# Optimization experiments

Hardware: AMD Instinct MI355X
Metric: run time of the kernel (lower is better)

Reference implementation:

```python
import jax, jax.numpy as jnp
import numpy as np

B, T, C = 8, 1024, 768
NH = 12
HD = C // NH  # 64


def setup_inputs() -> dict:
    key = jax.random.key(0)
    k1, k2, k3 = jax.random.split(key, 3)
    x = jax.random.normal(k1, (B, T, C), dtype=jnp.float32)
    w_attn = jax.random.normal(k2, (C, 3 * C), dtype=jnp.float32) * 0.02
    b_attn = jnp.zeros((3 * C,), dtype=jnp.float32)
    w_proj = jax.random.normal(k3, (C, C), dtype=jnp.float32) * 0.02
    b_proj = jnp.zeros((C,), dtype=jnp.float32)
    return {"x": x, "w_attn": w_attn, "b_attn": b_attn, "w_proj": w_proj, "b_proj": b_proj}


def reference(x, w_attn, b_attn, w_proj, b_proj):
    Bb, Tt, Cc = x.shape
    qkv = x @ w_attn + b_attn  # [B,T,3C]
    q, k, v = jnp.split(qkv, [Cc, 2 * Cc], axis=-1)
    # [B, NH, T, HD]
    q = q.reshape(Bb, Tt, NH, HD).swapaxes(1, 2)
    k = k.reshape(Bb, Tt, NH, HD).swapaxes(1, 2)
    v = v.reshape(Bb, Tt, NH, HD).swapaxes(1, 2)
    scale = 1.0 / jnp.sqrt(jnp.asarray(HD, dtype=x.dtype))
    att = jnp.einsum("bhqd,bhkd->bhqk", q, k) * scale  # [B,NH,T,T]
    causal = jnp.tril(jnp.ones((Tt, Tt), dtype=bool))[None, None]
    att = jnp.where(causal, att, jnp.asarray(-jnp.inf, dtype=att.dtype))
    att = jax.nn.softmax(att, axis=-1)
    y = jnp.einsum("bhqk,bhkd->bhqd", att, v)  # [B,NH,T,HD]
    y = y.swapaxes(1, 2).reshape(Bb, Tt, Cc)
    return y @ w_proj + b_proj
```

## Files before the change

### kernel.cpp

```cpp
#include <hip/hip_runtime.h>
#include <cstdint>
#include <cstddef>

typedef __attribute__((ext_vector_type(8))) short short8;
typedef __attribute__((ext_vector_type(4))) float f32x4;
typedef __attribute__((ext_vector_type(4))) unsigned short u16x4;

#define ASYNC16(gp, lp) \
  __builtin_amdgcn_global_load_lds((const __attribute__((address_space(1))) unsigned int*)(gp), \
                                   (__attribute__((address_space(3))) unsigned int*)(lp), 16, 0, 0)

__device__ __forceinline__ unsigned short f2b(float f) {
  union { float f; unsigned int u; } c; c.f = f;
  unsigned int u = c.u;
  return (unsigned short)((u + 0x7fffu + ((u >> 16) & 1u)) >> 16);
}


__global__ __launch_bounds__(256) void prep(
    const float* __restrict__ x, unsigned short* __restrict__ xb,
    const float* __restrict__ w_attn, unsigned short* __restrict__ waT,
    const float* __restrict__ w_proj, unsigned short* __restrict__ wpT) {
  __shared__ unsigned short Ts[64][65];
  const int bb = blockIdx.x;
  const int tid = threadIdx.x;
  if (bb < 3072) {
    int i = (bb * 256 + tid) * 8;
    float4 v0 = *(const float4*)(x + i);
    float4 v1 = *(const float4*)(x + i + 4);
    short8 v;
    ((unsigned short*)&v)[0] = f2b(v0.x);
    ((unsigned short*)&v)[1] = f2b(v0.y);
    ((unsigned short*)&v)[2] = f2b(v0.z);
    ((unsigned short*)&v)[3] = f2b(v0.w);
    ((unsigned short*)&v)[4] = f2b(v1.x);
    ((unsigned short*)&v)[5] = f2b(v1.y);
    ((unsigned short*)&v)[6] = f2b(v1.z);
    ((unsigned short*)&v)[7] = f2b(v1.w);
    *(short8*)(xb + i) = v;
    return;
  }
  const float* W; unsigned short* WT; int Kd, Nd, n0, k0;
  if (bb < 3504) {
    int t = bb - 3072; W = w_attn; WT = waT; Kd = 768; Nd = 2304;
    n0 = (t % 36) * 64; k0 = (t / 36) * 64;
  } else {
    int t = bb - 3504; W = w_proj; WT = wpT; Kd = 768; Nd = 768;
    n0 = (t % 12) * 64; k0 = (t / 12) * 64;
  }
  for (int idx = tid; idx < 4096; idx += 256) {
    int lr = idx >> 6, lc = idx & 63;
    Ts[lr][lc] = f2b(W[(size_t)(k0 + lr) * Nd + n0 + lc]);
  }
  __syncthreads();
  for (int idx = tid; idx < 4096; idx += 256) {
    int nr = idx >> 6, kc = idx & 63;
    WT[(size_t)(n0 + nr) * Kd + k0 + kc] = Ts[kc][nr];
  }
}


__global__ __launch_bounds__(256, 2) void gemm_qkv(
    const unsigned short* __restrict__ A,
    const unsigned short* __restrict__ Bt,
    const float* __restrict__ bias,
    unsigned short* __restrict__ q,
    unsigned short* __restrict__ k,
    unsigned short* __restrict__ vT)
{
  __shared__ unsigned short As[2][128 * 64];
  __shared__ unsigned short Bs[2][128 * 64];
  const int tid = threadIdx.x;
  const int w = tid >> 6, lane = tid & 63;
  const int wm = w >> 1, wn = w & 1;
  const int lr = lane & 15, lq = lane >> 4;

  const int bid = blockIdx.x;
  const int xcd = bid & 7;
  const int local = bid >> 3;
  const int ty = local >> 3;
  const int tx = xcd * 8 + (local & 7);
  const int m0 = tx * 128, n0 = ty * 128;
  const f32x4 fzero = {0.f, 0.f, 0.f, 0.f};

  f32x4 acc[4][4];
  for (int i = 0; i < 4; ++i) for (int j = 0; j < 4; ++j) acc[i][j] = fzero;

  const int trow = tid >> 3;
  const int tcol = (tid & 7) ^ (trow & 7);
  const unsigned short* Asrc = A + (size_t)(m0 + trow) * 768 + tcol * 8;
  const unsigned short* Bsrc = Bt + (size_t)(n0 + trow) * 768 + tcol * 8;
  const int dst0 = tid * 16;

#define STAGE_QKV(s, bidx) do { \
    const unsigned short* as_ = Asrc + (s) * 64; \
    const unsigned short* bs_ = Bsrc + (s) * 64; \
    ASYNC16(as_,            (char*)As[bidx] + dst0); \
    ASYNC16(as_ + 32 * 768, (char*)As[bidx] + dst0 + 4096); \
    ASYNC16(as_ + 64 * 768, (char*)As[bidx] + dst0 + 8192); \
    ASYNC16(as_ + 96 * 768, (char*)As[bidx] + dst0 + 12288); \
    ASYNC16(bs_,            (char*)Bs[bidx] + dst0); \
    ASYNC16(bs_ + 32 * 768, (char*)Bs[bidx] + dst0 + 4096); \
    ASYNC16(bs_ + 64 * 768, (char*)Bs[bidx] + dst0 + 8192); \
    ASYNC16(bs_ + 96 * 768, (char*)Bs[bidx] + dst0 + 12288); \
  } while (0)

  STAGE_QKV(0, 0);

  const int swz = (lq ^ (lr & 7)) * 16;
  const int arow = (wm * 64 + lr) * 128;
  const int brow = (wn * 64 + lr) * 128;

  for (int s = 0; s < 12; ++s) {
    __builtin_amdgcn_s_barrier();
    if (s + 1 < 12) {
      STAGE_QKV(s + 1, (s + 1) & 1);
      asm volatile("s_waitcnt vmcnt(8)" ::: "memory");
    } else {
      asm volatile("s_waitcnt vmcnt(0)" ::: "memory");
    }
    __builtin_amdgcn_s_barrier();
    __builtin_amdgcn_sched_barrier(0);
    const char* asb = (const char*)As[s & 1];
    const char* bsb = (const char*)Bs[s & 1];
    for (int ks = 0; ks < 2; ++ks) {
      const int cb = swz ^ (ks << 6);
      short8 a[4], b[4];
      for (int i = 0; i < 4; ++i)
        a[i] = *(const short8*)(asb + arow + i * 2048 + cb);
      for (int j = 0; j < 4; ++j)
        b[j] = *(const short8*)(bsb + brow + j * 2048 + cb);
      for (int i = 0; i < 4; ++i)
        for (int j = 0; j < 4; ++j)
          acc[i][j] = __builtin_amdgcn_mfma_f32_16x16x32_bf16(a[i], b[j], acc[i][j], 0, 0, 0);
    }
  }
#undef STAGE_QKV

  const int colbase = n0 + wn * 64;
  const int sec = colbase / 768;
  const float QSCALE = 0.18033688011112042f;
  for (int j = 0; j < 4; ++j) {
    int col = colbase + j * 16 + lr;
    int cc = col - sec * 768;
    int h = cc >> 6, d = cc & 63;
    float bv = bias[col];
    for (int i = 0; i < 4; ++i) {
      int row0 = m0 + wm * 64 + i * 16 + lq * 4;
      int bidx = row0 >> 10, t0 = row0 & 1023;
      int bh = bidx * 12 + h;
      if (sec == 0) {
        for (int r = 0; r < 4; ++r)
          q[((size_t)bh * 1024 + t0 + r) * 64 + d] = f2b((acc[i][j][r] + bv) * QSCALE);
      } else if (sec == 1) {
        for (int r = 0; r < 4; ++r)
          k[((size_t)bh * 1024 + t0 + r) * 64 + d] = f2b(acc[i][j][r] + bv);
      } else {
        u16x4 pv;
        pv[0] = f2b(acc[i][j][0] + bv);
        pv[1] = f2b(acc[i][j][1] + bv);
        pv[2] = f2b(acc[i][j][2] + bv);
        pv[3] = f2b(acc[i][j][3] + bv);
        *(u16x4*)(vT + ((size_t)bh * 64 + d) * 1024 + t0) = pv;
      }
    }
  }
}


__global__ __launch_bounds__(256, 3) void attn(
    const unsigned short* __restrict__ q,
    const unsigned short* __restrict__ kk,
    const unsigned short* __restrict__ vT,
    unsigned short* __restrict__ y)
{
  __shared__ __attribute__((aligned(16))) char smem[46080];
  unsigned short* KsB0 = (unsigned short*)smem;
  unsigned short* KsB1 = (unsigned short*)(smem + 9216);
  unsigned short* VtB0 = (unsigned short*)(smem + 18432);
  unsigned short* VtB1 = (unsigned short*)(smem + 27648);
  unsigned short* Ps   = (unsigned short*)(smem + 36864);
  unsigned short* Qs   = (unsigned short*)smem;

  const int tid = threadIdx.x;
  const int w = tid >> 6, lane = tid & 63;
  const int lr = lane & 15, lq = lane >> 4;

  const int bid = blockIdx.x;
  const int xcd = bid & 7;
  const int local = bid >> 3;
  const int bh = xcd + 8 * (local >> 3);
  const int qp = local & 7;
  const int qt1 = 15 - qp;
  const int b = bh / 12, h = bh - b * 12;
  const f32x4 fzero = {0.f, 0.f, 0.f, 0.f};

  unsigned short* Pw = Ps + w * 16 * 72;
  const unsigned short* kbase = kk + (size_t)bh * 65536;
  const unsigned short* vbase = vT + (size_t)bh * 65536;

  const int c0 = tid, c1 = tid + 256;
  short8 kreg[2], vreg[2];
  kreg[0] = *(const short8*)(kbase + (size_t)c0 * 8);
  kreg[1] = *(const short8*)(kbase + (size_t)c1 * 8);
  vreg[0] = *(const short8*)(vbase + (size_t)(c0 >> 3) * 1024 + (c0 & 7) * 8);
  vreg[1] = *(const short8*)(vbase + (size_t)(c1 >> 3) * 1024 + (c1 & 7) * 8);

  {
    const unsigned short* qa = q + ((size_t)bh * 1024 + qp * 64) * 64;
    const unsigned short* qb = q + ((size_t)bh * 1024 + qt1 * 64) * 64;
    for (int c = tid; c < 512; c += 256) {
      int row = c >> 3, d0 = (c & 7) * 8;
      *(short8*)(Qs + row * 72 + d0)        = *(const short8*)(qa + (size_t)c * 8);
      *(short8*)(Qs + (row + 64) * 72 + d0) = *(const short8*)(qb + (size_t)c * 8);
    }
  }
  __syncthreads();
  short8 qf0[2], qf1[2];
  for (int ks = 0; ks < 2; ++ks) {
    qf0[ks] = *(const short8*)(Qs + (w * 16 + lr) * 72 + ks * 32 + lq * 8);
    qf1[ks] = *(const short8*)(Qs + (64 + w * 16 + lr) * 72 + ks * 32 + lq * 8);
  }
  __syncthreads();

  const int wo0 = (c0 >> 3) * 72 + (c0 & 7) * 8;
  const int wo1 = (c1 >> 3) * 72 + (c1 & 7) * 8;

  *(short8*)(KsB0 + wo0) = kreg[0];
  *(short8*)(KsB0 + wo1) = kreg[1];
  *(short8*)(VtB0 + wo0) = vreg[0];
  *(short8*)(VtB0 + wo1) = vreg[1];

  const int nkt = qt1 + 1;
  {
    const unsigned short* kp = kbase + 4096;
    const unsigned short* vp = vbase + 64;
    kreg[0] = *(const short8*)(kp + (size_t)c0 * 8);
    kreg[1] = *(const short8*)(kp + (size_t)c1 * 8);
    vreg[0] = *(const short8*)(vp + (size_t)(c0 >> 3) * 1024 + (c0 & 7) * 8);
    vreg[1] = *(const short8*)(vp + (size_t)(c1 >> 3) * 1024 + (c1 & 7) * 8);
  }

  f32x4 o0[4], o1[4];
  float l0[4], l1[4];
  for (int jd = 0; jd < 4; ++jd) { o0[jd] = fzero; o1[jd] = fzero; }
  for (int r = 0; r < 4; ++r) { l0[r] = 0.0f; l1[r] = 0.0f; }

  for (int kt = 0; kt < nkt; ++kt) {
    __syncthreads();
    const unsigned short* Ks = (kt & 1) ? KsB1 : KsB0;
    const unsigned short* Vt = (kt & 1) ? VtB1 : VtB0;
    if (kt + 1 < nkt) {
      unsigned short* Ksn = (kt & 1) ? KsB0 : KsB1;
      unsigned short* Vtn = (kt & 1) ? VtB0 : VtB1;
      *(short8*)(Ksn + wo0) = kreg[0];
      *(short8*)(Ksn + wo1) = kreg[1];
      *(short8*)(Vtn + wo0) = vreg[0];
      *(short8*)(Vtn + wo1) = vreg[1];
      if (kt + 2 < nkt) {
        const unsigned short* kp = kbase + (size_t)(kt + 2) * 4096;
        const unsigned short* vp = vbase + (size_t)(kt + 2) * 64;
        kreg[0] = *(const short8*)(kp + (size_t)c0 * 8);
        kreg[1] = *(const short8*)(kp + (size_t)c1 * 8);
        vreg[0] = *(const short8*)(vp + (size_t)(c0 >> 3) * 1024 + (c0 & 7) * 8);
        vreg[1] = *(const short8*)(vp + (size_t)(c1 >> 3) * 1024 + (c1 & 7) * 8);
      }
    }

    const bool act0 = (kt <= qp);

    f32x4 s0[4], s1[4];
    for (int j = 0; j < 4; ++j) { s0[j] = fzero; s1[j] = fzero; }
    {
      short8 bk[2][4];
      for (int ks = 0; ks < 2; ++ks)
        for (int j = 0; j < 4; ++j)
          bk[ks][j] = *(const short8*)(Ks + (j * 16 + lr) * 72 + ks * 32 + lq * 8);
      __builtin_amdgcn_s_setprio(1);
      if (act0) {
        for (int ks = 0; ks < 2; ++ks)
          for (int j = 0; j < 4; ++j)
            s0[j] = __builtin_amdgcn_mfma_f32_16x16x32_bf16(qf0[ks], bk[ks][j], s0[j], 0, 0, 0);
      }
      for (int ks = 0; ks < 2; ++ks)
        for (int j = 0; j < 4; ++j)
          s1[j] = __builtin_amdgcn_mfma_f32_16x16x32_bf16(qf1[ks], bk[ks][j], s1[j], 0, 0, 0);
      __builtin_amdgcn_s_setprio(0);
    }

    short8 bvr[2][4];
    for (int ks = 0; ks < 2; ++ks)
      for (int jd = 0; jd < 4; ++jd)
        bvr[ks][jd] = *(const short8*)(Vt + (jd * 16 + lr) * 72 + ks * 32 + lq * 8);

    if (act0) {
      if (kt == qp) {
        int rowt = w * 16 + lq * 4;
        for (int j = 0; j < 4; ++j) {
          int colt = j * 16 + lr;
          for (int r = 0; r < 4; ++r)
            if (colt > rowt + r) s0[j][r] = -1e30f;
        }
      }
      for (int r = 0; r < 4; ++r) {
        int prow = (lq * 4 + r) * 72;
        float acc = 0.0f;
        for (int j = 0; j < 4; ++j) {
          float p = __builtin_amdgcn_exp2f(s0[j][r]);
          acc += p;
          union { float f; unsigned int u; } cv; cv.f = p;
          Pw[prow + j * 16 + lr] = (unsigned short)((cv.u + 0x8000u) >> 16);
        }
        l0[r] += acc;
      }
      __builtin_amdgcn_s_setprio(1);
      for (int ks = 0; ks < 2; ++ks) {
        short8 ap = *(const short8*)(Pw + lr * 72 + ks * 32 + lq * 8);
        for (int jd = 0; jd < 4; ++jd)
          o0[jd] = __builtin_amdgcn_mfma_f32_16x16x32_bf16(ap, bvr[ks][jd], o0[jd], 0, 0, 0);
      }
      __builtin_amdgcn_s_setprio(0);
    }

    {
      if (kt == qt1) {
        int rowt = w * 16 + lq * 4;
        for (int j = 0; j < 4; ++j) {
          int colt = j * 16 + lr;
          for (int r = 0; r < 4; ++r)
            if (colt > rowt + r) s1[j][r] = -1e30f;
        }
      }
      for (int r = 0; r < 4; ++r) {
        int prow = (lq * 4 + r) * 72;
        float acc = 0.0f;
        for (int j = 0; j < 4; ++j) {
          float p = __builtin_amdgcn_exp2f(s1[j][r]);
          acc += p;
          union { float f; unsigned int u; } cv; cv.f = p;
          Pw[prow + j * 16 + lr] = (unsigned short)((cv.u + 0x8000u) >> 16);
        }
        l1[r] += acc;
      }
      __builtin_amdgcn_s_setprio(1);
      for (int ks = 0; ks < 2; ++ks) {
        short8 ap = *(const short8*)(Pw + lr * 72 + ks * 32 + lq * 8);
        for (int jd = 0; jd < 4; ++jd)
          o1[jd] = __builtin_amdgcn_mfma_f32_16x16x32_bf16(ap, bvr[ks][jd], o1[jd], 0, 0, 0);
      }
      __builtin_amdgcn_s_setprio(0);
    }
  }

  for (int r = 0; r < 4; ++r) {
    float a0 = l0[r], a1 = l1[r];
    for (int off = 1; off < 16; off <<= 1) {
      a0 += __shfl_xor(a0, off, 16);
      a1 += __shfl_xor(a1, off, 16);
    }
    l0[r] = 1.0f / a0;
    l1[r] = 1.0f / a1;
  }
  int t0 = qp * 64 + w * 16 + lq * 4;
  int t1 = qt1 * 64 + w * 16 + lq * 4;
  for (int jd = 0; jd < 4; ++jd) {
    int d = jd * 16 + lr;
    for (int r = 0; r < 4; ++r) {
      y[((size_t)b * 1024 + t0 + r) * 768 + h * 64 + d] = f2b(o0[jd][r] * l0[r]);
      y[((size_t)b * 1024 + t1 + r) * 768 + h * 64 + d] = f2b(o1[jd][r] * l1[r]);
    }
  }
}


__global__ __launch_bounds__(256, 3) void gemm_proj(
    const unsigned short* __restrict__ A,
    const unsigned short* __restrict__ Bt,
    const float* __restrict__ bias,
    float* __restrict__ out)
{
  __shared__ unsigned short As[2][64 * 64];
  __shared__ unsigned short Bs[2][128 * 64];
  const int tid = threadIdx.x;
  const int w = tid >> 6, lane = tid & 63;
  const int wm = w >> 1, wn = w & 1;
  const int lr = lane & 15, lq = lane >> 4;

  const int bid = blockIdx.x;
  const int xcd = bid & 7;
  const int local = bid >> 3;
  const int ty = local >> 4;
  const int tx = xcd * 16 + (local & 15);
  const int m0 = tx * 64, n0 = ty * 128;
  const f32x4 fzero = {0.f, 0.f, 0.f, 0.f};

  f32x4 acc[2][4];
  for (int i = 0; i < 2; ++i) for (int j = 0; j < 4; ++j) acc[i][j] = fzero;

  const int trow = tid >> 3;
  const int tcol = (tid & 7) ^ (trow & 7);
  const unsigned short* Asrc = A + (size_t)(m0 + trow) * 768 + tcol * 8;
  const unsigned short* Bsrc = Bt + (size_t)(n0 + trow) * 768 + tcol * 8;
  const int dst0 = tid * 16;

#define STAGE_PROJ(s, bidx) do { \
    const unsigned short* as_ = Asrc + (s) * 64; \
    const unsigned short* bs_ = Bsrc + (s) * 64; \
    ASYNC16(as_,            (char*)As[bidx] + dst0); \
    ASYNC16(as_ + 32 * 768, (char*)As[bidx] + dst0 + 4096); \
    ASYNC16(bs_,            (char*)Bs[bidx] + dst0); \
    ASYNC16(bs_ + 32 * 768, (char*)Bs[bidx] + dst0 + 4096); \
    ASYNC16(bs_ + 64 * 768, (char*)Bs[bidx] + dst0 + 8192); \
    ASYNC16(bs_ + 96 * 768, (char*)Bs[bidx] + dst0 + 12288); \
  } while (0)

  STAGE_PROJ(0, 0);

  const int swz = (lq ^ (lr & 7)) * 16;
  const int arow = (wm * 32 + lr) * 128;
  const int brow = (wn * 64 + lr) * 128;

  for (int s = 0; s < 12; ++s) {
    __builtin_amdgcn_s_barrier();
    if (s + 1 < 12) {
      STAGE_PROJ(s + 1, (s + 1) & 1);
      asm volatile("s_waitcnt vmcnt(6)" ::: "memory");
    } else {
      asm volatile("s_waitcnt vmcnt(0)" ::: "memory");
    }
    __builtin_amdgcn_s_barrier();
    __builtin_amdgcn_sched_barrier(0);
    const char* asb = (const char*)As[s & 1];
    const char* bsb = (const char*)Bs[s & 1];
    for (int ks = 0; ks < 2; ++ks) {
      const int cb = swz ^ (ks << 6);
      short8 a[2], b[4];
      for (int i = 0; i < 2; ++i)
        a[i] = *(const short8*)(asb + arow + i * 2048 + cb);
      for (int j = 0; j < 4; ++j)
        b[j] = *(const short8*)(bsb + brow + j * 2048 + cb);
      for (int i = 0; i < 2; ++i)
        for (int j = 0; j < 4; ++j)
          acc[i][j] = __builtin_amdgcn_mfma_f32_16x16x32_bf16(a[i], b[j], acc[i][j], 0, 0, 0);
    }
  }
#undef STAGE_PROJ

  for (int j = 0; j < 4; ++j) {
    int col = n0 + wn * 64 + j * 16 + lr;
    float bv = bias[col];
    for (int i = 0; i < 2; ++i) {
      int row0 = m0 + wm * 32 + i * 16 + lq * 4;
      for (int r = 0; r < 4; ++r)
        out[(size_t)(row0 + r) * 768 + col] = acc[i][j][r] + bv;
    }
  }
}


extern "C" void kernel_launch(void* const* d_in, const int* in_sizes, int n_in,
                              void* d_out, int out_size, void* d_ws, size_t ws_size,
                              hipStream_t stream) {
  const float* x      = (const float*)d_in[0];
  const float* w_attn = (const float*)d_in[1];
  const float* b_attn = (const float*)d_in[2];
  const float* w_proj = (const float*)d_in[3];
  const float* b_proj = (const float*)d_in[4];
  float* out = (float*)d_out;

  char* p = (char*)d_ws;
  unsigned short* xb  = (unsigned short*)p; p += (size_t)8192 * 768 * 2;
  unsigned short* waT = (unsigned short*)p; p += (size_t)2304 * 768 * 2;
  unsigned short* wpT = (unsigned short*)p; p += (size_t)768 * 768 * 2;
  unsigned short* qb  = (unsigned short*)p; p += (size_t)96 * 1024 * 64 * 2;
  unsigned short* kb  = (unsigned short*)p; p += (size_t)96 * 1024 * 64 * 2;
  unsigned short* vTb = (unsigned short*)p; p += (size_t)96 * 64 * 1024 * 2;
  unsigned short* yb  = (unsigned short*)p; p += (size_t)8192 * 768 * 2;

  prep<<<3648, 256, 0, stream>>>(x, xb, w_attn, waT, w_proj, wpT);
  gemm_qkv<<<1152, 256, 0, stream>>>(xb, waT, b_attn, qb, kb, vTb);
  attn<<<768, 256, 0, stream>>>(qb, kb, vTb, yb);
  gemm_proj<<<768, 256, 0, stream>>>(yb, wpT, b_proj, out);
}
```

Before: 174.2 us.

## Split paired causal query tiles into one tile per block, single-buffer V

The attention kernel no longer pairs a short and a long causal query tile in one block; each block now handles a single 64-row query tile, so the grid doubles to 1536 blocks. V tiles are single-buffered and an extra barrier separates the softmax from the PV product, which cuts LDS use and allows four blocks per CU instead of three. The trade-off is that work per block now varies with the tile index, so load balance depends on the hardware scheduler. Each K/V tile is also loaded once per query tile rather than once per pair, and the extra barrier per iteration adds synchronisation.

```diff
diff --git a/kernel.cpp b/kernel.cpp
--- a/kernel.cpp
+++ b/kernel.cpp
@@ -168,18 +168,17 @@
 }
 
 
-__global__ __launch_bounds__(256, 3) void attn(
+__global__ __launch_bounds__(256, 4) void attn(
     const unsigned short* __restrict__ q,
     const unsigned short* __restrict__ kk,
     const unsigned short* __restrict__ vT,
     unsigned short* __restrict__ y)
 {
-  __shared__ __attribute__((aligned(16))) char smem[46080];
+  __shared__ __attribute__((aligned(16))) char smem[36864];
   unsigned short* KsB0 = (unsigned short*)smem;
   unsigned short* KsB1 = (unsigned short*)(smem + 9216);
-  unsigned short* VtB0 = (unsigned short*)(smem + 18432);
-  unsigned short* VtB1 = (unsigned short*)(smem + 27648);
-  unsigned short* Ps   = (unsigned short*)(smem + 36864);
+  unsigned short* Vt   = (unsigned short*)(smem + 18432);
+  unsigned short* Ps   = (unsigned short*)(smem + 27648);
   unsigned short* Qs   = (unsigned short*)smem;
 
   const int tid = threadIdx.x;
@@ -189,17 +188,20 @@
   const int bid = blockIdx.x;
   const int xcd = bid & 7;
   const int local = bid >> 3;
-  const int bh = xcd + 8 * (local >> 3);
-  const int qp = local & 7;
-  const int qt1 = 15 - qp;
+  const int bh = xcd + 8 * (local >> 4);
+  const int s = local & 15;
   const int b = bh / 12, h = bh - b * 12;
   const f32x4 fzero = {0.f, 0.f, 0.f, 0.f};
 
   unsigned short* Pw = Ps + w * 16 * 72;
   const unsigned short* kbase = kk + (size_t)bh * 65536;
   const unsigned short* vbase = vT + (size_t)bh * 65536;
+  const int nkt = s + 1;
 
   const int c0 = tid, c1 = tid + 256;
+  const int wo0 = (c0 >> 3) * 72 + (c0 & 7) * 8;
+  const int wo1 = (c1 >> 3) * 72 + (c1 & 7) * 8;
+
   short8 kreg[2], vreg[2];
   kreg[0] = *(const short8*)(kbase + (size_t)c0 * 8);
   kreg[1] = *(const short8*)(kbase + (size_t)c1 * 8);
@@ -207,168 +209,101 @@
   vreg[1] = *(const short8*)(vbase + (size_t)(c1 >> 3) * 1024 + (c1 & 7) * 8);
 
   {
-    const unsigned short* qa = q + ((size_t)bh * 1024 + qp * 64) * 64;
-    const unsigned short* qb = q + ((size_t)bh * 1024 + qt1 * 64) * 64;
+    const unsigned short* qa = q + ((size_t)bh * 1024 + s * 64) * 64;
     for (int c = tid; c < 512; c += 256) {
       int row = c >> 3, d0 = (c & 7) * 8;
-      *(short8*)(Qs + row * 72 + d0)        = *(const short8*)(qa + (size_t)c * 8);
-      *(short8*)(Qs + (row + 64) * 72 + d0) = *(const short8*)(qb + (size_t)c * 8);
+      *(short8*)(Qs + row * 72 + d0) = *(const short8*)(qa + (size_t)c * 8);
     }
   }
   __syncthreads();
-  short8 qf0[2], qf1[2];
-  for (int ks = 0; ks < 2; ++ks) {
-    qf0[ks] = *(const short8*)(Qs + (w * 16 + lr) * 72 + ks * 32 + lq * 8);
-    qf1[ks] = *(const short8*)(Qs + (64 + w * 16 + lr) * 72 + ks * 32 + lq * 8);
-  }
+  short8 qf[2];
+  qf[0] = *(const short8*)(Qs + (w * 16 + lr) * 72 + lq * 8);
+  qf[1] = *(const short8*)(Qs + (w * 16 + lr) * 72 + 32 + lq * 8);
   __syncthreads();
-
-  const int wo0 = (c0 >> 3) * 72 + (c0 & 7) * 8;
-  const int wo1 = (c1 >> 3) * 72 + (c1 & 7) * 8;
 
   *(short8*)(KsB0 + wo0) = kreg[0];
   *(short8*)(KsB0 + wo1) = kreg[1];
-  *(short8*)(VtB0 + wo0) = vreg[0];
-  *(short8*)(VtB0 + wo1) = vreg[1];
-
-  const int nkt = qt1 + 1;
-  {
-    const unsigned short* kp = kbase + 4096;
-    const unsigned short* vp = vbase + 64;
-    kreg[0] = *(const short8*)(kp + (size_t)c0 * 8);
-    kreg[1] = *(const short8*)(kp + (size_t)c1 * 8);
-    vreg[0] = *(const short8*)(vp + (size_t)(c0 >> 3) * 1024 + (c0 & 7) * 8);
-    vreg[1] = *(const short8*)(vp + (size_t)(c1 >> 3) * 1024 + (c1 & 7) * 8);
-  }
-
-  f32x4 o0[4], o1[4];
-  float l0[4], l1[4];
-  for (int jd = 0; jd < 4; ++jd) { o0[jd] = fzero; o1[jd] = fzero; }
-  for (int r = 0; r < 4; ++r) { l0[r] = 0.0f; l1[r] = 0.0f; }
+  if (nkt > 1) {
+    kreg[0] = *(const short8*)(kbase + 4096 + (size_t)c0 * 8);
+    kreg[1] = *(const short8*)(kbase + 4096 + (size_t)c1 * 8);
+  }
+
+  f32x4 o[4];
+  float l[4];
+  for (int jd = 0; jd < 4; ++jd) o[jd] = fzero;
+  for (int r = 0; r < 4; ++r) l[r] = 0.0f;
 
   for (int kt = 0; kt < nkt; ++kt) {
     __syncthreads();
-    const unsigned short* Ks = (kt & 1) ? KsB1 : KsB0;
-    const unsigned short* Vt = (kt & 1) ? VtB1 : VtB0;
+    *(short8*)(Vt + wo0) = vreg[0];
+    *(short8*)(Vt + wo1) = vreg[1];
     if (kt + 1 < nkt) {
-      unsigned short* Ksn = (kt & 1) ? KsB0 : KsB1;
-      unsigned short* Vtn = (kt & 1) ? VtB0 : VtB1;
-      *(short8*)(Ksn + wo0) = kreg[0];
-      *(short8*)(Ksn + wo1) = kreg[1];
-      *(short8*)(Vtn + wo0) = vreg[0];
-      *(short8*)(Vtn + wo1) = vreg[1];
+      unsigned short* Kn = (kt & 1) ? KsB0 : KsB1;
+      *(short8*)(Kn + wo0) = kreg[0];
+      *(short8*)(Kn + wo1) = kreg[1];
+      const unsigned short* vp = vbase + (size_t)(kt + 1) * 64;
+      vreg[0] = *(const short8*)(vp + (size_t)(c0 >> 3) * 1024 + (c0 & 7) * 8);
+      vreg[1] = *(const short8*)(vp + (size_t)(c1 >> 3) * 1024 + (c1 & 7) * 8);
       if (kt + 2 < nkt) {
         const unsigned short* kp = kbase + (size_t)(kt + 2) * 4096;
-        const unsigned short* vp = vbase + (size_t)(kt + 2) * 64;
         kreg[0] = *(const short8*)(kp + (size_t)c0 * 8);
         kreg[1] = *(const short8*)(kp + (size_t)c1 * 8);
-        vreg[0] = *(const short8*)(vp + (size_t)(c0 >> 3) * 1024 + (c0 & 7) * 8);
-        vreg[1] = *(const short8*)(vp + (size_t)(c1 >> 3) * 1024 + (c1 & 7) * 8);
-      }
-    }
-
-    const bool act0 = (kt <= qp);
-
-    f32x4 s0[4], s1[4];
-    for (int j = 0; j < 4; ++j) { s0[j] = fzero; s1[j] = fzero; }
-    {
-      short8 bk[2][4];
-      for (int ks = 0; ks < 2; ++ks)
-        for (int j = 0; j < 4; ++j)
-          bk[ks][j] = *(const short8*)(Ks + (j * 16 + lr) * 72 + ks * 32 + lq * 8);
-      __builtin_amdgcn_s_setprio(1);
-      if (act0) {
-        for (int ks = 0; ks < 2; ++ks)
-          for (int j = 0; j < 4; ++j)
-            s0[j] = __builtin_amdgcn_mfma_f32_16x16x32_bf16(qf0[ks], bk[ks][j], s0[j], 0, 0, 0);
-      }
-      for (int ks = 0; ks < 2; ++ks)
-        for (int j = 0; j < 4; ++j)
-          s1[j] = __builtin_amdgcn_mfma_f32_16x16x32_bf16(qf1[ks], bk[ks][j], s1[j], 0, 0, 0);
-      __builtin_amdgcn_s_setprio(0);
-    }
-
-    short8 bvr[2][4];
+      }
+    }
+
+    const unsigned short* Ks = (kt & 1) ? KsB1 : KsB0;
+    f32x4 sv[4];
+    for (int j = 0; j < 4; ++j) sv[j] = fzero;
+    __builtin_amdgcn_s_setprio(1);
     for (int ks = 0; ks < 2; ++ks)
-      for (int jd = 0; jd < 4; ++jd)
-        bvr[ks][jd] = *(const short8*)(Vt + (jd * 16 + lr) * 72 + ks * 32 + lq * 8);
-
-    if (act0) {
-      if (kt == qp) {
-        int rowt = w * 16 + lq * 4;
-        for (int j = 0; j < 4; ++j) {
-          int colt = j * 16 + lr;
-          for (int r = 0; r < 4; ++r)
-            if (colt > rowt + r) s0[j][r] = -1e30f;
-        }
-      }
-      for (int r = 0; r < 4; ++r) {
-        int prow = (lq * 4 + r) * 72;
-        float acc = 0.0f;
-        for (int j = 0; j < 4; ++j) {
-          float p = __builtin_amdgcn_exp2f(s0[j][r]);
-          acc += p;
-          union { float f; unsigned int u; } cv; cv.f = p;
-          Pw[prow + j * 16 + lr] = (unsigned short)((cv.u + 0x8000u) >> 16);
-        }
-        l0[r] += acc;
-      }
-      __builtin_amdgcn_s_setprio(1);
-      for (int ks = 0; ks < 2; ++ks) {
-        short8 ap = *(const short8*)(Pw + lr * 72 + ks * 32 + lq * 8);
-        for (int jd = 0; jd < 4; ++jd)
-          o0[jd] = __builtin_amdgcn_mfma_f32_16x16x32_bf16(ap, bvr[ks][jd], o0[jd], 0, 0, 0);
-      }
-      __builtin_amdgcn_s_setprio(0);
-    }
-
-    {
-      if (kt == qt1) {
-        int rowt = w * 16 + lq * 4;
-        for (int j = 0; j < 4; ++j) {
-          int colt = j * 16 + lr;
-          for (int r = 0; r < 4; ++r)
-            if (colt > rowt + r) s1[j][r] = -1e30f;
-        }
-      }
-      for (int r = 0; r < 4; ++r) {
-        int prow = (lq * 4 + r) * 72;
-        float acc = 0.0f;
-        for (int j = 0; j < 4; ++j) {
-          float p = __builtin_amdgcn_exp2f(s1[j][r]);
-          acc += p;
-          union { float f; unsigned int u; } cv; cv.f = p;
-          Pw[prow + j * 16 + lr] = (unsigned short)((cv.u + 0x8000u) >> 16);
-        }
-        l1[r] += acc;
-      }
-      __builtin_amdgcn_s_setprio(1);
-      for (int ks = 0; ks < 2; ++ks) {
-        short8 ap = *(const short8*)(Pw + lr * 72 + ks * 32 + lq * 8);
-        for (int jd = 0; jd < 4; ++jd)
-          o1[jd] = __builtin_amdgcn_mfma_f32_16x16x32_bf16(ap, bvr[ks][jd], o1[jd], 0, 0, 0);
-      }
-      __builtin_amdgcn_s_setprio(0);
-    }
+      for (int j = 0; j < 4; ++j) {
+        short8 bk = *(const short8*)(Ks + (j * 16 + lr) * 72 + ks * 32 + lq * 8);
+        sv[j] = __builtin_amdgcn_mfma_f32_16x16x32_bf16(qf[ks], bk, sv[j], 0, 0, 0);
+      }
+    __builtin_amdgcn_s_setprio(0);
+
+    if (kt == s) {
+      int rowt = w * 16 + lq * 4;
+      for (int j = 0; j < 4; ++j) {
+        int colt = j * 16 + lr;
+        for (int r = 0; r < 4; ++r)
+          if (colt > rowt + r) sv[j][r] = -1e30f;
+      }
+    }
+    for (int r = 0; r < 4; ++r) {
+      int prow = (lq * 4 + r) * 72;
+      float acc = 0.0f;
+      for (int j = 0; j < 4; ++j) {
+        float p = __builtin_amdgcn_exp2f(sv[j][r]);
+        acc += p;
+        union { float f; unsigned int u; } cv; cv.f = p;
+        Pw[prow + j * 16 + lr] = (unsigned short)((cv.u + 0x8000u) >> 16);
+      }
+      l[r] += acc;
+    }
+    __syncthreads();
+    __builtin_amdgcn_s_setprio(1);
+    for (int ks = 0; ks < 2; ++ks) {
+      short8 ap = *(const short8*)(Pw + lr * 72 + ks * 32 + lq * 8);
+      for (int jd = 0; jd < 4; ++jd) {
+        short8 bv = *(const short8*)(Vt + (jd * 16 + lr) * 72 + ks * 32 + lq * 8);
+        o[jd] = __builtin_amdgcn_mfma_f32_16x16x32_bf16(ap, bv, o[jd], 0, 0, 0);
+      }
+    }
+    __builtin_amdgcn_s_setprio(0);
   }
 
   for (int r = 0; r < 4; ++r) {
-    float a0 = l0[r], a1 = l1[r];
-    for (int off = 1; off < 16; off <<= 1) {
+    float a0 = l[r];
+    for (int off = 1; off < 16; off <<= 1)
       a0 += __shfl_xor(a0, off, 16);
-      a1 += __shfl_xor(a1, off, 16);
-    }
-    l0[r] = 1.0f / a0;
-    l1[r] = 1.0f / a1;
-  }
-  int t0 = qp * 64 + w * 16 + lq * 4;
-  int t1 = qt1 * 64 + w * 16 + lq * 4;
+    l[r] = 1.0f / a0;
+  }
+  int t0 = s * 64 + w * 16 + lq * 4;
   for (int jd = 0; jd < 4; ++jd) {
     int d = jd * 16 + lr;
-    for (int r = 0; r < 4; ++r) {
-      y[((size_t)b * 1024 + t0 + r) * 768 + h * 64 + d] = f2b(o0[jd][r] * l0[r]);
-      y[((size_t)b * 1024 + t1 + r) * 768 + h * 64 + d] = f2b(o1[jd][r] * l1[r]);
-    }
+    for (int r = 0; r < 4; ++r)
+      y[((size_t)b * 1024 + t0 + r) * 768 + h * 64 + d] = f2b(o[jd][r] * l[r]);
   }
 }
 
@@ -479,6 +414,6 @@
 
   prep<<<3648, 256, 0, stream>>>(x, xb, w_attn, waT, w_proj, wpT);
   gemm_qkv<<<1152, 256, 0, stream>>>(xb, waT, b_attn, qb, kb, vTb);
-  attn<<<768, 256, 0, stream>>>(qb, kb, vTb, yb);
+  attn<<<1536, 256, 0, stream>>>(qb, kb, vTb, yb);
   gemm_proj<<<768, 256, 0, stream>>>(yb, wpT, b_proj, out);
 }
```

New measurement: 184.2 us. 5.8% more time.
